# Kernel tuning notes

Hardware: AMD Instinct MI355X
Metric: run time of the kernel (lower is better)

The kernel has to match this reference:

```python
import jax, jax.numpy as jnp
import numpy as np

NQ, N, C = 8192, 32768, 128


def setup_inputs() -> dict:
    key = jax.random.key(0)
    k1, k2, k3 = jax.random.split(key, 3)
    return {
        "query_pos": jax.random.normal(k1, (NQ, 3), dtype=jnp.float32),
        "neural_feat": jax.random.normal(k2, (N, C), dtype=jnp.float32),
        "neural_pos": jax.random.normal(k3, (N, 3), dtype=jnp.float32),
        "knn": 64,
    }


def _cdist(a, b):
    # Euclidean pairwise distances via the (|a|^2 + |b|^2 - 2ab) expansion.
    a2 = jnp.sum(a * a, axis=-1, keepdims=True)          # [N',1]
    b2 = jnp.sum(b * b, axis=-1)                          # [N]
    d2 = a2 + b2[None, :] - 2.0 * (a @ b.T)               # [N',N]
    return jnp.sqrt(jnp.maximum(d2, 1e-12))


def reference(query_pos, neural_feat, neural_pos, knn):
    dists = _cdist(query_pos, neural_pos)                 # [N',N]
    # torch.topk(largest=False, sorted=True) == top_k of negated dists.
    neg_vals, closest_ind = jax.lax.top_k(-dists, knn)    # [N',k]
    closest_dists = -neg_vals                             # ascending
    closest_feat = neural_feat[closest_ind]               # [N',k,C] gather
    inv_dist = 1.0 / (closest_dists + 1e-5)               # [N',k]
    retrieved_feat = jnp.sum(closest_feat * inv_dist[..., None], axis=1)  # [N',C]
    return retrieved_feat
```

## Files before the change

kernel.cpp:

```cpp
#include <hip/hip_runtime.h>
#include <math.h>

#define NQ    8192
#define NPTS  32768
#define KNN   64
#define QPB   4
#define CAPW  56
#define NBLK  (NQ / QPB)
#define PPW   (NPTS / 4)
#define NGRP  (PPW / 256)
#define MAXM  224

__device__ __forceinline__ unsigned key_of(float f) {
  unsigned u = __float_as_uint(f);
  return (u & 0x80000000u) ? ~u : (u | 0x80000000u);
}
__device__ __forceinline__ float val_of(unsigned k) {
  unsigned u = (k & 0x80000000u) ? (k & 0x7fffffffu) : ~k;
  return __uint_as_float(u);
}
__device__ __forceinline__ int mbcnt64(unsigned long long m) {
  return __builtin_amdgcn_mbcnt_hi((unsigned)(m >> 32),
         __builtin_amdgcn_mbcnt_lo((unsigned)m, 0));
}
__device__ __forceinline__ float rflf(float x) {
  return __int_as_float(__builtin_amdgcn_readfirstlane(__float_as_int(x)));
}
__device__ __forceinline__ int rfli(int x) { return __builtin_amdgcn_readfirstlane(x); }

__device__ __forceinline__ float norm_cdf(float x) { return 0.5f * erfcf(-x * 0.70710678f); }
__device__ __forceinline__ float ball_mass(float mu, float r) {
  float a = r - mu, b = r + mu;
  float e = __expf(-0.5f * b * b) - __expf(-0.5f * a * a);
  return e / (mu * 2.50662827f) + norm_cdf(a) - norm_cdf(-mu) + norm_cdf(b) - norm_cdf(mu);
}

__global__ __launch_bounds__(256, 8) void ft_knn_kernel(
    const float* __restrict__ qpos, const float* __restrict__ feat,
    const float* __restrict__ pos, float* __restrict__ out) {

  __shared__ uint2 sCand[QPB][4][CAPW];
  __shared__ uint2 sSel[QPB][KNN];
  __shared__ int   sCntW[4][QPB];
  __shared__ float sQ[QPB][4];
  __shared__ float sTau[QPB], sTlo[QPB], sThi[QPB];
  __shared__ int   sAct[QPB], sAny;

  const int tid   = threadIdx.x;
  const int lane  = tid & 63;
  const int wv    = tid >> 6;
  const int qbase = blockIdx.x * QPB;

  if (tid < QPB) {
    int gq = qbase + tid;
    float x = qpos[gq * 3 + 0], y = qpos[gq * 3 + 1], z = qpos[gq * 3 + 2];
    float b = x * x + y * y + z * z;
    sQ[tid][0] = -2.f * x; sQ[tid][1] = -2.f * y; sQ[tid][2] = -2.f * z; sQ[tid][3] = b;
    float mu = fmaxf(sqrtf(b), 0.05f);
    const float target = 110.0f / 32768.0f;
    float lo = 0.f, hi = mu + 8.f;
    for (int i = 0; i < 16; ++i) {
      float r = 0.5f * (lo + hi);
      if (ball_mass(mu, r) < target) lo = r; else hi = r;
    }
    sTau[tid] = hi * hi;
    sTlo[tid] = 0.f; sThi[tid] = -1.f;
    sAct[tid] = 1;
  }
  __syncthreads();

  for (int attempt = 0; attempt < 12; ++attempt) {
    float qx[QPB], qy[QPB], qz[QPB], bq[QPB], tq[QPB]; int act[QPB], cnt[QPB];
    #pragma unroll
    for (int q = 0; q < QPB; ++q) {
      qx[q] = rflf(sQ[q][0]); qy[q] = rflf(sQ[q][1]); qz[q] = rflf(sQ[q][2]);
      bq[q] = rflf(sQ[q][3]);
      act[q] = rfli(sAct[q]);
      float tau = rflf(sTau[q]);
      tq[q] = act[q] ? (tau - bq[q]) : -1e30f;
      cnt[q] = 0;
    }
    if (act[0] | act[1] | act[2] | act[3]) {
      const int pw = wv * PPW;
      for (int g = 0; g < NGRP; ++g) {
        const int pt = pw + g * 256 + lane * 4;
        const float* bp = pos + (size_t)pt * 3;
        const float4 A  = *(const float4*)(bp);
        const float4 B  = *(const float4*)(bp + 4);
        const float4 Cc = *(const float4*)(bp + 8);
        const float x0 = A.x,  y0 = A.y,  z0 = A.z;
        const float x1 = A.w,  y1 = B.x,  z1 = B.y;
        const float x2 = B.z,  y2 = B.w,  z2 = Cc.x;
        const float x3 = Cc.y, y3 = Cc.z, z3 = Cc.w;
        const float n0 = x0 * x0 + y0 * y0 + z0 * z0;
        const float n1 = x1 * x1 + y1 * y1 + z1 * z1;
        const float n2 = x2 * x2 + y2 * y2 + z2 * z2;
        const float n3 = x3 * x3 + y3 * y3 + z3 * z3;
        #pragma unroll
        for (int q = 0; q < QPB; ++q) {
          float d0 = fmaf(z0, qz[q], fmaf(y0, qy[q], fmaf(x0, qx[q], n0)));
          float d1 = fmaf(z1, qz[q], fmaf(y1, qy[q], fmaf(x1, qx[q], n1)));
          float d2 = fmaf(z2, qz[q], fmaf(y2, qy[q], fmaf(x2, qx[q], n2)));
          float d3 = fmaf(z3, qz[q], fmaf(y3, qy[q], fmaf(x3, qx[q], n3)));
          const bool h0 = d0 < tq[q], h1 = d1 < tq[q], h2 = d2 < tq[q], h3 = d3 < tq[q];
          const unsigned long long m0 = __ballot(h0), m1 = __ballot(h1),
                                   m2 = __ballot(h2), m3 = __ballot(h3);
          if (m0) { int p = cnt[q] + mbcnt64(m0);
                    if (h0 && p < CAPW) sCand[q][wv][p] = make_uint2(key_of(d0 + bq[q]), (unsigned)(pt + 0));
                    cnt[q] += (int)__popcll(m0); }
          if (m1) { int p = cnt[q] + mbcnt64(m1);
                    if (h1 && p < CAPW) sCand[q][wv][p] = make_uint2(key_of(d1 + bq[q]), (unsigned)(pt + 1));
                    cnt[q] += (int)__popcll(m1); }
          if (m2) { int p = cnt[q] + mbcnt64(m2);
                    if (h2 && p < CAPW) sCand[q][wv][p] = make_uint2(key_of(d2 + bq[q]), (unsigned)(pt + 2));
                    cnt[q] += (int)__popcll(m2); }
          if (m3) { int p = cnt[q] + mbcnt64(m3);
                    if (h3 && p < CAPW) sCand[q][wv][p] = make_uint2(key_of(d3 + bq[q]), (unsigned)(pt + 3));
                    cnt[q] += (int)__popcll(m3); }
        }
      }
    }
    __syncthreads();
    if (lane == 0) {
      #pragma unroll
      for (int q = 0; q < QPB; ++q) if (act[q]) sCntW[wv][q] = cnt[q];
    }
    if (tid == 0) sAny = 0;
    __syncthreads();
    if (tid < QPB && sAct[tid]) {
      int tot = 0, ovf = 0;
      #pragma unroll
      for (int w = 0; w < 4; ++w) { int c = sCntW[w][tid]; ovf |= (c > CAPW); tot += c; }
      if (!ovf && tot >= KNN && tot <= MAXM) sAct[tid] = 0;
      else {
        if (!ovf && tot < KNN) { sTlo[tid] = sTau[tid];
          sTau[tid] = (sThi[tid] < 0.f) ? sTau[tid] * 3.f : 0.5f * (sTau[tid] + sThi[tid]); }
        else { sThi[tid] = sTau[tid]; sTau[tid] = 0.5f * (sTlo[tid] + sTau[tid]); }
        sAny = 1;
      }
    }
    __syncthreads();
    if (!sAny) break;
  }

  {
    const int q = wv;
    const int c0 = rfli(min(sCntW[0][q], CAPW));
    const int c1 = rfli(min(sCntW[1][q], CAPW));
    const int c2 = rfli(min(sCntW[2][q], CAPW));
    const int c3 = rfli(min(sCntW[3][q], CAPW));
    const int P1 = c0, P2 = P1 + c1, P3 = P2 + c2, m = P3 + c3;

    unsigned k[4], id[4];
    #pragma unroll
    for (int s = 0; s < 4; ++s) {
      const int g = s * 64 + lane;
      const int ge1 = g >= P1, ge2 = g >= P2, ge3 = g >= P3;
      const int w = ge1 + ge2 + ge3;
      const int sb = ge3 ? P3 : (ge2 ? P2 : (ge1 ? P1 : 0));
      uint2 kv = make_uint2(0xFFFFFFFFu, 0u);
      if (g < m) kv = sCand[q][w][g - sb];
      k[s] = kv.x; id[s] = kv.y;
    }

    unsigned lo = 0u, hi = 0xFFFFFFFFu;
    for (int it = 0; it < 32; ++it) {
      unsigned mid = lo + ((hi - lo) >> 1);
      int c = (int)(__popcll(__ballot(k[0] <= mid)) + __popcll(__ballot(k[1] <= mid)) +
                    __popcll(__ballot(k[2] <= mid)) + __popcll(__ballot(k[3] <= mid)));
      if (c >= KNN) hi = mid; else lo = mid + 1;
    }
    const unsigned K = lo;

    int fill = 0;
    #pragma unroll
    for (int s = 0; s < 4; ++s) {
      const bool lt = k[s] < K;
      const unsigned long long msk = __ballot(lt);
      if (msk) {
        const int p = fill + mbcnt64(msk);
        if (lt) { float dv = val_of(k[s]);
                  float w_ = 1.f / (sqrtf(fmaxf(dv, 1e-12f)) + 1e-5f);
                  sSel[q][p] = make_uint2(id[s], __float_as_uint(w_)); }
        fill += (int)__popcll(msk);
      }
    }
    #pragma unroll
    for (int s = 0; s < 4; ++s) {
      const bool eq = (k[s] == K);
      const unsigned long long msk = __ballot(eq);
      if (msk) {
        const int p = fill + mbcnt64(msk);
        if (eq && p < KNN) { float dv = val_of(k[s]);
                             float w_ = 1.f / (sqrtf(fmaxf(dv, 1e-12f)) + 1e-5f);
                             sSel[q][p] = make_uint2(id[s], __float_as_uint(w_)); }
        fill += (int)__popcll(msk);
      }
    }
  }

  {
    const int q = wv, gq = qbase + wv;
    float ax = 0.f, ay = 0.f;
    #pragma unroll 8
    for (int j = 0; j < KNN; ++j) {
      const uint2 pr = sSel[q][j];
      const float w = __uint_as_float(pr.y);
      const float2 f2 = *(const float2*)(feat + ((size_t)pr.x << 7) + (lane << 1));
      ax = fmaf(w, f2.x, ax);
      ay = fmaf(w, f2.y, ay);
    }
    *(float2*)(out + ((size_t)gq << 7) + (lane << 1)) = make_float2(ax, ay);
  }
}

extern "C" void kernel_launch(void* const* d_in, const int* in_sizes, int n_in,
                              void* d_out, int out_size, void* d_ws, size_t ws_size,
                              hipStream_t stream) {
  const float* qpos = (const float*)d_in[0];
  const float* feat = (const float*)d_in[1];
  const float* pos  = (const float*)d_in[2];
  float* out = (float*)d_out;
  ft_knn_kernel<<<dim3(NBLK), dim3(256), 0, stream>>>(qpos, feat, pos, out);
}
```

Before: 143.5 us.

## Bin points into a uniform grid and search only cells within each query's radius

Adds a preprocessing pipeline: count points per cell of a 16^3 grid over [-4,4], prefix-scan the counts, and scatter the points into cell-sorted SoA arrays in the workspace. Per-query thresholds are also computed in a separate kernel. The main kernel uses one wavefront per query and scans only the grid rows that overlap the radius ball, instead of brute-forcing all 32768 points. This removes most of the distance work, at the cost of four extra launches, atomics and gathered workspace reads. The old brute-force kernel stays as a fallback when the workspace is too small.

Measured after the change: 159.6 us. 11.2% more time.

```diff
diff --git a/kernel.cpp b/kernel.cpp
--- a/kernel.cpp
+++ b/kernel.cpp
@@ -4,6 +4,219 @@
 #define NQ    8192
 #define NPTS  32768
 #define KNN   64
+#define GRIDD 16
+#define NCELL 4096
+#define CAP   224
+
+#define WS_CNT   0
+#define WS_START 4096
+#define WS_TAU   8704
+#define WS_X     16896
+#define WS_Y     49664
+#define WS_Z     82432
+#define WS_I     115200
+#define WS_TOTAL 147968
+
+__device__ __forceinline__ int mbcnt64(unsigned long long m) {
+  return __builtin_amdgcn_mbcnt_hi((unsigned)(m >> 32),
+         __builtin_amdgcn_mbcnt_lo((unsigned)m, 0));
+}
+__device__ __forceinline__ int cell1(float v) {
+  int c = (int)floorf((v + 4.f) * 2.f);
+  return min(GRIDD - 1, max(0, c));
+}
+__device__ __forceinline__ float norm_cdf(float x) { return 0.5f * erfcf(-x * 0.70710678f); }
+__device__ __forceinline__ float ball_mass(float mu, float r) {
+  float a = r - mu, b = r + mu;
+  float e = __expf(-0.5f * b * b) - __expf(-0.5f * a * a);
+  return e / (mu * 2.50662827f) + norm_cdf(a) - norm_cdf(-mu) + norm_cdf(b) - norm_cdf(mu);
+}
+
+__global__ void k_count_tau(const float* __restrict__ qpos, const float* __restrict__ pos,
+                            int* __restrict__ cnt, float* __restrict__ tau) {
+  const int b = blockIdx.x;
+  if (b < 32) {
+    const int q = b * 256 + threadIdx.x;
+    float x = qpos[3 * q], y = qpos[3 * q + 1], z = qpos[3 * q + 2];
+    float b2 = x * x + y * y + z * z;
+    float mu = fmaxf(sqrtf(b2), 0.05f);
+    const float target = 110.0f / 32768.0f;
+    float lo = 0.f, hi = mu + 8.f;
+    for (int i = 0; i < 20; ++i) {
+      float r = 0.5f * (lo + hi);
+      if (ball_mass(mu, r) < target) lo = r; else hi = r;
+    }
+    tau[q] = hi * hi;
+  } else {
+    const int p = (b - 32) * 256 + threadIdx.x;
+    float x = pos[3 * p], y = pos[3 * p + 1], z = pos[3 * p + 2];
+    int c = (cell1(z) * GRIDD + cell1(y)) * GRIDD + cell1(x);
+    atomicAdd(&cnt[c], 1);
+  }
+}
+
+__global__ void k_scan(int* __restrict__ cnt, int* __restrict__ start) {
+  __shared__ int wsum[4];
+  const int tid = threadIdx.x, lane = tid & 63, wv = tid >> 6;
+  int loc[16]; int s = 0;
+  #pragma unroll
+  for (int i = 0; i < 16; ++i) { loc[i] = cnt[tid * 16 + i]; s += loc[i]; }
+  int sc = s;
+  #pragma unroll
+  for (int d = 1; d < 64; d <<= 1) { int t = __shfl_up(sc, d, 64); if (lane >= d) sc += t; }
+  if (lane == 63) wsum[wv] = sc;
+  __syncthreads();
+  int wpre = 0;
+  for (int w = 0; w < wv; ++w) wpre += wsum[w];
+  int excl = wpre + sc - s;
+  #pragma unroll
+  for (int i = 0; i < 16; ++i) { start[tid * 16 + i] = excl; cnt[tid * 16 + i] = excl; excl += loc[i]; }
+  if (tid == 255) start[NCELL] = excl;
+}
+
+__global__ void k_scatter(const float* __restrict__ pos, int* __restrict__ cursor,
+                          float* __restrict__ X, float* __restrict__ Y, float* __restrict__ Z,
+                          int* __restrict__ I) {
+  const int p = blockIdx.x * 256 + threadIdx.x;
+  float x = pos[3 * p], y = pos[3 * p + 1], z = pos[3 * p + 2];
+  int c = (cell1(z) * GRIDD + cell1(y)) * GRIDD + cell1(x);
+  int j = atomicAdd(&cursor[c], 1);
+  X[j] = x; Y[j] = y; Z[j] = z; I[j] = p;
+}
+
+__global__ __launch_bounds__(256, 8) void k_main(
+    const float* __restrict__ qpos, const float* __restrict__ feat,
+    const float* __restrict__ tauA, const int* __restrict__ start,
+    const float* __restrict__ X, const float* __restrict__ Y, const float* __restrict__ Z,
+    const int* __restrict__ I, float* __restrict__ out) {
+
+  __shared__ uint2 sCand[4][CAP];
+  __shared__ uint2 sSel[4][KNN];
+
+  const int tid = threadIdx.x, lane = tid & 63, wv = tid >> 6;
+  const int gq  = blockIdx.x * 4 + wv;
+
+  const float qx = qpos[3 * gq], qy = qpos[3 * gq + 1], qz = qpos[3 * gq + 2];
+  float tau = tauA[gq];
+  float tlo = 0.f, thi = -1.f;
+  int m = 0;
+
+  for (int attempt = 0; attempt < 16; ++attempt) {
+    m = 0;
+    const float r = sqrtf(tau);
+    const int xlo = cell1(qx - r), xhi = cell1(qx + r);
+    const int ylo = cell1(qy - r), yhi = cell1(qy + r);
+    const int zlo = cell1(qz - r), zhi = cell1(qz + r);
+    for (int cz = zlo; cz <= zhi; ++cz) {
+      for (int cy = ylo; cy <= yhi; ++cy) {
+        const int row = (cz * GRIDD + cy) * GRIDD;
+        const int rs = start[row + xlo];
+        const int re = start[row + xhi + 1];
+        for (int j0 = rs; j0 < re; j0 += 64) {
+          const int j = j0 + lane;
+          float d = 3.4e38f;
+          if (j < re) {
+            float dx = X[j] - qx, dy = Y[j] - qy, dz = Z[j] - qz;
+            d = fmaf(dx, dx, fmaf(dy, dy, dz * dz));
+          }
+          const bool h = d < tau;
+          const unsigned long long msk = __ballot(h);
+          if (msk) {
+            const int p = m + mbcnt64(msk);
+            if (h && p < CAP) sCand[wv][p] = make_uint2(__float_as_uint(d), (unsigned)I[j]);
+            m += (int)__popcll(msk);
+          }
+        }
+      }
+    }
+    if (m >= KNN && m <= CAP) break;
+    if (m < KNN) { tlo = tau; tau = (thi < 0.f) ? tau * 2.5f : 0.5f * (tau + thi); }
+    else         { thi = tau; tau = 0.5f * (tlo + tau); }
+  }
+
+  const int mm = min(m, CAP);
+  const int NS = (mm + 63) >> 6;
+  unsigned k[4], id[4];
+  #pragma unroll
+  for (int s = 0; s < 4; ++s) {
+    k[s] = 0xFFFFFFFFu; id[s] = 0u;
+    if (s < NS) {
+      const int g = s * 64 + lane;
+      if (g < mm) { uint2 kv = sCand[wv][g]; k[s] = kv.x; id[s] = kv.y; }
+    }
+  }
+  sSel[wv][lane] = make_uint2(0u, 0u);
+
+  if (mm > KNN) {
+    unsigned lo = 0u, hi = __float_as_uint(tau);
+    while (lo < hi) {
+      const unsigned mid = lo + ((hi - lo) >> 1);
+      int c = 0;
+      #pragma unroll
+      for (int s = 0; s < 4; ++s)
+        if (s < NS) c += (int)__popcll(__ballot(k[s] <= mid));
+      if (c >= KNN) hi = mid; else lo = mid + 1;
+    }
+    const unsigned K = lo;
+    int fill = 0;
+    #pragma unroll
+    for (int s = 0; s < 4; ++s) {
+      if (s < NS) {
+        const bool lt = k[s] < K;
+        const unsigned long long msk = __ballot(lt);
+        if (msk) {
+          const int p = fill + mbcnt64(msk);
+          if (lt) {
+            float dv = __uint_as_float(k[s]);
+            float w_ = 1.f / (sqrtf(fmaxf(dv, 1e-12f)) + 1e-5f);
+            sSel[wv][p] = make_uint2(id[s], __float_as_uint(w_));
+          }
+          fill += (int)__popcll(msk);
+        }
+      }
+    }
+    #pragma unroll
+    for (int s = 0; s < 4; ++s) {
+      if (s < NS) {
+        const bool eq = (k[s] == K);
+        const unsigned long long msk = __ballot(eq);
+        if (msk) {
+          const int p = fill + mbcnt64(msk);
+          if (eq && p < KNN) {
+            float dv = __uint_as_float(k[s]);
+            float w_ = 1.f / (sqrtf(fmaxf(dv, 1e-12f)) + 1e-5f);
+            sSel[wv][p] = make_uint2(id[s], __float_as_uint(w_));
+          }
+          fill += (int)__popcll(msk);
+        }
+      }
+    }
+  } else {
+    #pragma unroll
+    for (int s = 0; s < 4; ++s) {
+      if (s < NS) {
+        const int g = s * 64 + lane;
+        if (g < mm) {
+          float dv = __uint_as_float(k[s]);
+          float w_ = 1.f / (sqrtf(fmaxf(dv, 1e-12f)) + 1e-5f);
+          sSel[wv][g] = make_uint2(id[s], __float_as_uint(w_));
+        }
+      }
+    }
+  }
+
+  float ax = 0.f, ay = 0.f;
+  #pragma unroll 8
+  for (int j = 0; j < KNN; ++j) {
+    const uint2 pr = sSel[wv][j];
+    const float w = __uint_as_float(pr.y);
+    const float2 f2 = *(const float2*)(feat + ((size_t)pr.x << 7) + (lane << 1));
+    ax = fmaf(w, f2.x, ax);
+    ay = fmaf(w, f2.y, ay);
+  }
+  *(float2*)(out + ((size_t)gq << 7) + (lane << 1)) = make_float2(ax, ay);
+}
+
 #define QPB   4
 #define CAPW  56
 #define NBLK  (NQ / QPB)
@@ -19,41 +232,25 @@
   unsigned u = (k & 0x80000000u) ? (k & 0x7fffffffu) : ~k;
   return __uint_as_float(u);
 }
-__device__ __forceinline__ int mbcnt64(unsigned long long m) {
-  return __builtin_amdgcn_mbcnt_hi((unsigned)(m >> 32),
-         __builtin_amdgcn_mbcnt_lo((unsigned)m, 0));
-}
 __device__ __forceinline__ float rflf(float x) {
   return __int_as_float(__builtin_amdgcn_readfirstlane(__float_as_int(x)));
 }
 __device__ __forceinline__ int rfli(int x) { return __builtin_amdgcn_readfirstlane(x); }
 
-__device__ __forceinline__ float norm_cdf(float x) { return 0.5f * erfcf(-x * 0.70710678f); }
-__device__ __forceinline__ float ball_mass(float mu, float r) {
-  float a = r - mu, b = r + mu;
-  float e = __expf(-0.5f * b * b) - __expf(-0.5f * a * a);
-  return e / (mu * 2.50662827f) + norm_cdf(a) - norm_cdf(-mu) + norm_cdf(b) - norm_cdf(mu);
-}
-
-__global__ __launch_bounds__(256, 8) void ft_knn_kernel(
+__global__ __launch_bounds__(256, 8) void ft_knn_fallback(
     const float* __restrict__ qpos, const float* __restrict__ feat,
     const float* __restrict__ pos, float* __restrict__ out) {
-
   __shared__ uint2 sCand[QPB][4][CAPW];
   __shared__ uint2 sSel[QPB][KNN];
   __shared__ int   sCntW[4][QPB];
   __shared__ float sQ[QPB][4];
   __shared__ float sTau[QPB], sTlo[QPB], sThi[QPB];
   __shared__ int   sAct[QPB], sAny;
-
-  const int tid   = threadIdx.x;
-  const int lane  = tid & 63;
-  const int wv    = tid >> 6;
+  const int tid = threadIdx.x, lane = tid & 63, wv = tid >> 6;
   const int qbase = blockIdx.x * QPB;
-
   if (tid < QPB) {
     int gq = qbase + tid;
-    float x = qpos[gq * 3 + 0], y = qpos[gq * 3 + 1], z = qpos[gq * 3 + 2];
+    float x = qpos[gq * 3], y = qpos[gq * 3 + 1], z = qpos[gq * 3 + 2];
     float b = x * x + y * y + z * z;
     sQ[tid][0] = -2.f * x; sQ[tid][1] = -2.f * y; sQ[tid][2] = -2.f * z; sQ[tid][3] = b;
     float mu = fmaxf(sqrtf(b), 0.05f);
@@ -63,39 +260,28 @@
       float r = 0.5f * (lo + hi);
       if (ball_mass(mu, r) < target) lo = r; else hi = r;
     }
-    sTau[tid] = hi * hi;
-    sTlo[tid] = 0.f; sThi[tid] = -1.f;
-    sAct[tid] = 1;
+    sTau[tid] = hi * hi; sTlo[tid] = 0.f; sThi[tid] = -1.f; sAct[tid] = 1;
   }
   __syncthreads();
-
   for (int attempt = 0; attempt < 12; ++attempt) {
     float qx[QPB], qy[QPB], qz[QPB], bq[QPB], tq[QPB]; int act[QPB], cnt[QPB];
     #pragma unroll
     for (int q = 0; q < QPB; ++q) {
       qx[q] = rflf(sQ[q][0]); qy[q] = rflf(sQ[q][1]); qz[q] = rflf(sQ[q][2]);
-      bq[q] = rflf(sQ[q][3]);
-      act[q] = rfli(sAct[q]);
+      bq[q] = rflf(sQ[q][3]); act[q] = rfli(sAct[q]);
       float tau = rflf(sTau[q]);
-      tq[q] = act[q] ? (tau - bq[q]) : -1e30f;
-      cnt[q] = 0;
+      tq[q] = act[q] ? (tau - bq[q]) : -1e30f; cnt[q] = 0;
     }
     if (act[0] | act[1] | act[2] | act[3]) {
       const int pw = wv * PPW;
       for (int g = 0; g < NGRP; ++g) {
         const int pt = pw + g * 256 + lane * 4;
         const float* bp = pos + (size_t)pt * 3;
-        const float4 A  = *(const float4*)(bp);
-        const float4 B  = *(const float4*)(bp + 4);
-        const float4 Cc = *(const float4*)(bp + 8);
-        const float x0 = A.x,  y0 = A.y,  z0 = A.z;
-        const float x1 = A.w,  y1 = B.x,  z1 = B.y;
-        const float x2 = B.z,  y2 = B.w,  z2 = Cc.x;
-        const float x3 = Cc.y, y3 = Cc.z, z3 = Cc.w;
-        const float n0 = x0 * x0 + y0 * y0 + z0 * z0;
-        const float n1 = x1 * x1 + y1 * y1 + z1 * z1;
-        const float n2 = x2 * x2 + y2 * y2 + z2 * z2;
-        const float n3 = x3 * x3 + y3 * y3 + z3 * z3;
+        const float4 A = *(const float4*)(bp), B = *(const float4*)(bp + 4), Cc = *(const float4*)(bp + 8);
+        const float x0 = A.x, y0 = A.y, z0 = A.z, x1 = A.w, y1 = B.x, z1 = B.y;
+        const float x2 = B.z, y2 = B.w, z2 = Cc.x, x3 = Cc.y, y3 = Cc.z, z3 = Cc.w;
+        const float n0 = x0*x0+y0*y0+z0*z0, n1 = x1*x1+y1*y1+z1*z1;
+        const float n2 = x2*x2+y2*y2+z2*z2, n3 = x3*x3+y3*y3+z3*z3;
         #pragma unroll
         for (int q = 0; q < QPB; ++q) {
           float d0 = fmaf(z0, qz[q], fmaf(y0, qy[q], fmaf(x0, qx[q], n0)));
@@ -103,27 +289,18 @@
           float d2 = fmaf(z2, qz[q], fmaf(y2, qy[q], fmaf(x2, qx[q], n2)));
           float d3 = fmaf(z3, qz[q], fmaf(y3, qy[q], fmaf(x3, qx[q], n3)));
           const bool h0 = d0 < tq[q], h1 = d1 < tq[q], h2 = d2 < tq[q], h3 = d3 < tq[q];
-          const unsigned long long m0 = __ballot(h0), m1 = __ballot(h1),
-                                   m2 = __ballot(h2), m3 = __ballot(h3);
-          if (m0) { int p = cnt[q] + mbcnt64(m0);
-                    if (h0 && p < CAPW) sCand[q][wv][p] = make_uint2(key_of(d0 + bq[q]), (unsigned)(pt + 0));
-                    cnt[q] += (int)__popcll(m0); }
-          if (m1) { int p = cnt[q] + mbcnt64(m1);
-                    if (h1 && p < CAPW) sCand[q][wv][p] = make_uint2(key_of(d1 + bq[q]), (unsigned)(pt + 1));
-                    cnt[q] += (int)__popcll(m1); }
-          if (m2) { int p = cnt[q] + mbcnt64(m2);
-                    if (h2 && p < CAPW) sCand[q][wv][p] = make_uint2(key_of(d2 + bq[q]), (unsigned)(pt + 2));
-                    cnt[q] += (int)__popcll(m2); }
-          if (m3) { int p = cnt[q] + mbcnt64(m3);
-                    if (h3 && p < CAPW) sCand[q][wv][p] = make_uint2(key_of(d3 + bq[q]), (unsigned)(pt + 3));
-                    cnt[q] += (int)__popcll(m3); }
+          const unsigned long long m0 = __ballot(h0), m1 = __ballot(h1), m2 = __ballot(h2), m3 = __ballot(h3);
+          if (m0) { int p = cnt[q] + mbcnt64(m0); if (h0 && p < CAPW) sCand[q][wv][p] = make_uint2(key_of(d0 + bq[q]), (unsigned)(pt)); cnt[q] += (int)__popcll(m0); }
+          if (m1) { int p = cnt[q] + mbcnt64(m1); if (h1 && p < CAPW) sCand[q][wv][p] = make_uint2(key_of(d1 + bq[q]), (unsigned)(pt + 1)); cnt[q] += (int)__popcll(m1); }
+          if (m2) { int p = cnt[q] + mbcnt64(m2); if (h2 && p < CAPW) sCand[q][wv][p] = make_uint2(key_of(d2 + bq[q]), (unsigned)(pt + 2)); cnt[q] += (int)__popcll(m2); }
+          if (m3) { int p = cnt[q] + mbcnt64(m3); if (h3 && p < CAPW) sCand[q][wv][p] = make_uint2(key_of(d3 + bq[q]), (unsigned)(pt + 3)); cnt[q] += (int)__popcll(m3); }
         }
       }
     }
     __syncthreads();
     if (lane == 0) {
       #pragma unroll
-      for (int q = 0; q < QPB; ++q) if (act[q]) sCntW[wv][q] = cnt[q];
+      for (int q = 0; q < QPB; ++q) { if (act[q]) sCntW[wv][q] = cnt[q]; }
     }
     if (tid == 0) sAny = 0;
     __syncthreads();
@@ -142,15 +319,11 @@
     __syncthreads();
     if (!sAny) break;
   }
-
   {
     const int q = wv;
-    const int c0 = rfli(min(sCntW[0][q], CAPW));
-    const int c1 = rfli(min(sCntW[1][q], CAPW));
-    const int c2 = rfli(min(sCntW[2][q], CAPW));
-    const int c3 = rfli(min(sCntW[3][q], CAPW));
+    const int c0 = rfli(min(sCntW[0][q], CAPW)), c1 = rfli(min(sCntW[1][q], CAPW));
+    const int c2 = rfli(min(sCntW[2][q], CAPW)), c3 = rfli(min(sCntW[3][q], CAPW));
     const int P1 = c0, P2 = P1 + c1, P3 = P2 + c2, m = P3 + c3;
-
     unsigned k[4], id[4];
     #pragma unroll
     for (int s = 0; s < 4; ++s) {
@@ -162,7 +335,6 @@
       if (g < m) kv = sCand[q][w][g - sb];
       k[s] = kv.x; id[s] = kv.y;
     }
-
     unsigned lo = 0u, hi = 0xFFFFFFFFu;
     for (int it = 0; it < 32; ++it) {
       unsigned mid = lo + ((hi - lo) >> 1);
@@ -171,34 +343,26 @@
       if (c >= KNN) hi = mid; else lo = mid + 1;
     }
     const unsigned K = lo;
-
     int fill = 0;
     #pragma unroll
     for (int s = 0; s < 4; ++s) {
       const bool lt = k[s] < K;
       const unsigned long long msk = __ballot(lt);
-      if (msk) {
-        const int p = fill + mbcnt64(msk);
-        if (lt) { float dv = val_of(k[s]);
-                  float w_ = 1.f / (sqrtf(fmaxf(dv, 1e-12f)) + 1e-5f);
+      if (msk) { const int p = fill + mbcnt64(msk);
+        if (lt) { float dv = val_of(k[s]); float w_ = 1.f / (sqrtf(fmaxf(dv, 1e-12f)) + 1e-5f);
                   sSel[q][p] = make_uint2(id[s], __float_as_uint(w_)); }
-        fill += (int)__popcll(msk);
-      }
+        fill += (int)__popcll(msk); }
     }
     #pragma unroll
     for (int s = 0; s < 4; ++s) {
       const bool eq = (k[s] == K);
       const unsigned long long msk = __ballot(eq);
-      if (msk) {
-        const int p = fill + mbcnt64(msk);
-        if (eq && p < KNN) { float dv = val_of(k[s]);
-                             float w_ = 1.f / (sqrtf(fmaxf(dv, 1e-12f)) + 1e-5f);
+      if (msk) { const int p = fill + mbcnt64(msk);
+        if (eq && p < KNN) { float dv = val_of(k[s]); float w_ = 1.f / (sqrtf(fmaxf(dv, 1e-12f)) + 1e-5f);
                              sSel[q][p] = make_uint2(id[s], __float_as_uint(w_)); }
-        fill += (int)__popcll(msk);
-      }
-    }
-  }
-
+        fill += (int)__popcll(msk); }
+    }
+  }
   {
     const int q = wv, gq = qbase + wv;
     float ax = 0.f, ay = 0.f;
@@ -221,5 +385,23 @@
   const float* feat = (const float*)d_in[1];
   const float* pos  = (const float*)d_in[2];
   float* out = (float*)d_out;
-  ft_knn_kernel<<<dim3(NBLK), dim3(256), 0, stream>>>(qpos, feat, pos, out);
-}
+
+  if (ws_size >= (size_t)WS_TOTAL * 4) {
+    float* wsf = (float*)d_ws;
+    int*   wsi = (int*)d_ws;
+    int*   cnt   = wsi + WS_CNT;
+    int*   start = wsi + WS_START;
+    float* tau   = wsf + WS_TAU;
+    float* X     = wsf + WS_X;
+    float* Y     = wsf + WS_Y;
+    float* Z     = wsf + WS_Z;
+    int*   I     = wsi + WS_I;
+    (void)hipMemsetAsync(cnt, 0, NCELL * sizeof(int), stream);
+    k_count_tau<<<dim3(160), dim3(256), 0, stream>>>(qpos, pos, cnt, tau);
+    k_scan<<<dim3(1), dim3(256), 0, stream>>>(cnt, start);
+    k_scatter<<<dim3(128), dim3(256), 0, stream>>>(pos, cnt, X, Y, Z, I);
+    k_main<<<dim3(NQ / 4), dim3(256), 0, stream>>>(qpos, feat, tau, start, X, Y, Z, I, out);
+  } else {
+    ft_knn_fallback<<<dim3(NBLK), dim3(256), 0, stream>>>(qpos, feat, pos, out);
+  }
+}
```
